# Kernel tuning notes

Measured on AMD Instinct MI355X. Metric: run time of the kernel, lower is better.

## Reference

```python
import jax, jax.numpy as jnp
import numpy as np

NUM_HEADS = 12

def setup_inputs() -> dict:
    key = jax.random.key(0)
    k1, k2, k3 = jax.random.split(key, 3)
    B, N, C = 8, 1024, 768
    x = jax.random.normal(k1, (B, N, C), dtype=jnp.float32)
    Wqkv = jax.random.normal(k2, (C, 3 * C), dtype=jnp.float32) * (C ** -0.5)
    bqkv = jnp.zeros((3 * C,), dtype=jnp.float32)
    Wproj = jax.random.normal(k3, (C, C), dtype=jnp.float32) * (C ** -0.5)
    bproj = jnp.zeros((C,), dtype=jnp.float32)
    return {"x": x, "Wqkv": Wqkv, "bqkv": bqkv, "Wproj": Wproj, "bproj": bproj}

def reference(x, Wqkv, bqkv, Wproj, bproj):
    B, N, C = x.shape
    H = NUM_HEADS
    D = C // H
    scale = D ** -0.5
    qkv = x @ Wqkv + bqkv                       # [B,N,3C]
    qkv = qkv.reshape(B, N, 3, H, D)
    q, k, v = qkv[:, :, 0], qkv[:, :, 1], qkv[:, :, 2]  # [B,N,H,D]
    attn = jnp.einsum('bnhd,bmhd->bhnm', q, k) * scale  # [B,H,N,N]
    attn = jax.nn.softmax(attn, axis=-1)
    # dropout is identity in eval mode
    out = jnp.einsum('bhnm,bmhd->bnhd', attn, v).reshape(B, N, C)
    out = out @ Wproj + bproj
    return out
```

## Files before the change

kernel.cpp:

```cpp
#include <hip/hip_runtime.h>
#include <hip/hip_bf16.h>
#include <cstdint>
#include <cstddef>

typedef __bf16 bf16;
typedef __bf16 bf16x8 __attribute__((ext_vector_type(8)));
typedef __bf16 bf16x4 __attribute__((ext_vector_type(4)));
typedef __bf16 bf16x2 __attribute__((ext_vector_type(2)));
typedef float f32x4 __attribute__((ext_vector_type(4)));
typedef float f32x16 __attribute__((ext_vector_type(16)));
typedef unsigned int u32;
typedef u32 u32x4 __attribute__((ext_vector_type(4)));

#define LDS_CAST(p) (__attribute__((address_space(3))) void*)(p)
#define GLB_CAST(p) (const __attribute__((address_space(1))) void*)(p)
#define MFMA16(a, b, c) __builtin_amdgcn_mfma_f32_16x16x32_bf16(a, b, c, 0, 0, 0)
#define MFMA32(a, b, c) __builtin_amdgcn_mfma_f32_32x32x16_bf16(a, b, c, 0, 0, 0)

#if __has_builtin(__builtin_amdgcn_exp2f)
#define EXPF(x) __builtin_amdgcn_exp2f(x)
#define QK_SCALE 0.18033688011112042f
#else
#define EXPF(x) __expf(x)
#define QK_SCALE 0.125f
#endif

static constexpr int BATCH = 8;
static constexpr int NSEQ  = 1024;
static constexpr int CDIM  = 768;
static constexpr int NH    = 12;
static constexpr int HD    = 64;
static constexpr int MTOT  = BATCH * NSEQ;
static constexpr int NC3   = 3 * CDIM;

__device__ inline u32 pkbf(float a, float b) {
    bf16x2 t = { (bf16)a, (bf16)b };
    return __builtin_bit_cast(u32, t);
}

__global__ void cast_kernel(const float* __restrict__ src, bf16* __restrict__ dst, int n4) {
    int i = blockIdx.x * blockDim.x + threadIdx.x;
    if (i < n4) {
        float4 v = ((const float4*)src)[i];
        bf16x4 o = { (bf16)v.x, (bf16)v.y, (bf16)v.z, (bf16)v.w };
        ((bf16x4*)dst)[i] = o;
    }
}

__global__ void tcast_kernel(const float* __restrict__ src, bf16* __restrict__ dst,
                             int K, int N) {
    __shared__ float tile[32][33];
    const int n0 = blockIdx.x * 32, k0 = blockIdx.y * 32;
    const int tx = threadIdx.x & 31, ty = threadIdx.x >> 5;
#pragma unroll
    for (int p = 0; p < 4; p++)
        tile[ty + p * 8][tx] = src[(size_t)(k0 + ty + p * 8) * N + n0 + tx];
    __syncthreads();
#pragma unroll
    for (int p = 0; p < 4; p++)
        dst[(size_t)(n0 + ty + p * 8) * K + k0 + tx] = (bf16)tile[tx][ty + p * 8];
}

template <int MODE>
__global__ __launch_bounds__(512, 4) void gemm_kernel(
    const bf16* __restrict__ A, const bf16* __restrict__ Bt,
    const float* __restrict__ bias, float* __restrict__ outf,
    bf16* __restrict__ q, bf16* __restrict__ kk, bf16* __restrict__ v,
    int Ndim, int K)
{
    __shared__ alignas(16) bf16 sAB[3][12288];
    const int tid  = threadIdx.x;
    const int lane = tid & 63;
    const int quad = lane >> 4;
    const int l16  = lane & 15;
    const int wid  = tid >> 6;
    const int wmI  = wid >> 1;
    const int wnI  = wid & 1;

    const int wg = blockIdx.x;
    const int x  = (wg & 7) * (gridDim.x >> 3) + (wg >> 3);
    const int nTn = Ndim >> 7;
    const int tn = x % nTn, tm = x / nTn;
    const int tmB = tm << 8, tnB = tn << 7;

    int aoff[4], boff[4];
    {
        const int xr = ((quad ^ (l16 & 3)) << 3);
#pragma unroll
        for (int i = 0; i < 4; i++) aoff[i] = (wmI * 64 + i * 16 + l16) * 32 + xr;
#pragma unroll
        for (int j = 0; j < 4; j++) boff[j] = 8192 + (wnI * 64 + j * 16 + l16) * 32 + xr;
    }

    const int r0 = tid >> 2;
    const int c0 = (tid & 3) ^ (r0 & 3);
    const bf16* gA0 = A  + (size_t)(tmB + r0) * K + c0 * 8;
    const bf16* gA1 = gA0 + (size_t)128 * K;
    const bf16* gB0 = Bt + (size_t)(tnB + r0) * K + c0 * 8;
    const int ldsb = (tid & 448) * 8;

    auto STAGE = [&](int t, int bsel) {
        const int k0 = t << 5;
        bf16* d = &sAB[bsel][0];
        __builtin_amdgcn_global_load_lds(GLB_CAST(gA0 + k0), LDS_CAST(d + ldsb),        16, 0, 0);
        __builtin_amdgcn_global_load_lds(GLB_CAST(gA1 + k0), LDS_CAST(d + 4096 + ldsb), 16, 0, 0);
        __builtin_amdgcn_global_load_lds(GLB_CAST(gB0 + k0), LDS_CAST(d + 8192 + ldsb), 16, 0, 0);
    };

    const f32x4 fzero = {0.f, 0.f, 0.f, 0.f};
    f32x4 acc[4][4];
#pragma unroll
    for (int i = 0; i < 4; i++)
#pragma unroll
        for (int j = 0; j < 4; j++) acc[i][j] = fzero;

    const int NT = K >> 5;
    STAGE(0, 0);
    STAGE(1, 1);
    asm volatile("s_waitcnt vmcnt(3)" ::: "memory");
    __builtin_amdgcn_sched_barrier(0);
    __builtin_amdgcn_s_barrier();

    int bsel = 0;
    for (int t = 0; t < NT; ++t) {
        int b2 = bsel + 2; if (b2 >= 3) b2 -= 3;
        if (t + 2 < NT) STAGE(t + 2, b2);

        const bf16* buf = &sAB[bsel][0];
        bf16x8 af[4], bfr[4];
#pragma unroll
        for (int i = 0; i < 4; i++) af[i]  = *(const bf16x8*)(buf + aoff[i]);
#pragma unroll
        for (int j = 0; j < 4; j++) bfr[j] = *(const bf16x8*)(buf + boff[j]);

        __builtin_amdgcn_s_setprio(1);
#pragma unroll
        for (int i = 0; i < 4; i++)
#pragma unroll
            for (int j = 0; j < 4; j++) acc[i][j] = MFMA16(af[i], bfr[j], acc[i][j]);
        __builtin_amdgcn_s_setprio(0);

        if (t < NT - 1) {
            if (t + 2 < NT) asm volatile("s_waitcnt vmcnt(3)" ::: "memory");
            else            asm volatile("s_waitcnt vmcnt(0)" ::: "memory");
            __builtin_amdgcn_sched_barrier(0);
            __builtin_amdgcn_s_barrier();
            __builtin_amdgcn_sched_barrier(0);
        }
        bsel += 1; if (bsel >= 3) bsel -= 3;
    }

    if (MODE == 0) {
#pragma unroll
        for (int i = 0; i < 4; i++) {
            int row = tmB + wmI * 64 + i * 16 + quad * 4;
#pragma unroll
            for (int j = 0; j < 4; j++) {
                int col = tnB + wnI * 64 + j * 16 + l16;
                float bv = bias[col];
                float* op = outf + (size_t)row * Ndim + col;
#pragma unroll
                for (int r = 0; r < 4; r++) op[(size_t)r * Ndim] = acc[i][j][r] + bv;
            }
        }
    } else {
#pragma unroll
        for (int i = 0; i < 4; i++) {
            int row = tmB + wmI * 64 + i * 16 + quad * 4;
            int b  = row >> 10;
            int ns = row & 1023;
#pragma unroll
            for (int j = 0; j < 4; j++) {
                int col = tnB + wnI * 64 + j * 16 + l16;
                int t3  = col / 768;
                int rem = col - t3 * 768;
                int h = rem >> 6;
                int d = rem & 63;
                float bv = bias[col];
                if (t3 == 0) {
                    bf16* qp = q + ((size_t)(b * NH + h) * NSEQ + ns) * HD + d;
#pragma unroll
                    for (int r = 0; r < 4; r++)
                        qp[(size_t)r * HD] = (bf16)((acc[i][j][r] + bv) * (float)QK_SCALE);
                } else if (t3 == 1) {
                    bf16* kp = kk + ((size_t)(b * NH + h) * NSEQ + ns) * HD + d;
#pragma unroll
                    for (int r = 0; r < 4; r++) kp[(size_t)r * HD] = (bf16)(acc[i][j][r] + bv);
                } else {
                    bf16x4 pv = { (bf16)(acc[i][j][0] + bv), (bf16)(acc[i][j][1] + bv),
                                  (bf16)(acc[i][j][2] + bv), (bf16)(acc[i][j][3] + bv) };
                    *(bf16x4*)(v + ((size_t)(b * NH + h) * HD + d) * NSEQ + ns) = pv;
                }
            }
        }
    }
}

__global__ __launch_bounds__(256) void attn_kernel(
    const bf16* __restrict__ q, const bf16* __restrict__ k,
    const bf16* __restrict__ v, bf16* __restrict__ o)
{
    __shared__ alignas(16) bf16 sQ[128 * 64];
    __shared__ alignas(16) bf16 sK[2][64 * 64];
    __shared__ alignas(16) bf16 sV[2][64 * 64];
    const int tid  = threadIdx.x;
    const int lane = tid & 63;
    const int w    = tid >> 6;
    const int h    = lane >> 5;
    const int l32  = lane & 31;
    const int qt = blockIdx.x;
    const int bh = blockIdx.y;
    const int b = bh / NH, hh = bh - b * NH;

    const bf16* qb = q + ((size_t)bh * NSEQ + qt * 128) * HD;
    const bf16* kb = k + (size_t)bh * NSEQ * HD;
    const bf16* vb = v + (size_t)bh * HD * NSEQ;

#pragma unroll
    for (int i = 0; i < 4; i++) {
        int slot = w * 256 + i * 64 + lane;
        int r = slot >> 3, cs = slot & 7;
        __builtin_amdgcn_global_load_lds(GLB_CAST(qb + r * HD + ((cs ^ (r & 7)) * 8)),
                                         LDS_CAST(sQ + (w * 256 + i * 64) * 8), 16, 0, 0);
    }
    auto stageKV = [&](int kt, int buf) {
#pragma unroll
        for (int i = 0; i < 2; i++) {
            int slot = w * 128 + i * 64 + lane;
            int r = slot >> 3, cs = slot & 7;
            int cc = (cs ^ (r & 7)) * 8;
            __builtin_amdgcn_global_load_lds(GLB_CAST(kb + (size_t)(kt * 64 + r) * HD + cc),
                                             LDS_CAST(&sK[buf][(w * 128 + i * 64) * 8]), 16, 0, 0);
            __builtin_amdgcn_global_load_lds(GLB_CAST(vb + (size_t)r * NSEQ + kt * 64 + cc),
                                             LDS_CAST(&sV[buf][(w * 128 + i * 64) * 8]), 16, 0, 0);
        }
    };
    stageKV(0, 0);
    __syncthreads();

    bf16x8 qf[4];
    {
        int row = w * 32 + l32, rx = row & 7;
#pragma unroll
        for (int cd = 0; cd < 4; cd++)
            qf[cd] = *(const bf16x8*)(sQ + (row * 8 + ((2 * cd + h) ^ rx)) * 8);
    }

    f32x16 accO[2];
#pragma unroll
    for (int dt = 0; dt < 2; dt++)
#pragma unroll
        for (int i = 0; i < 16; i++) accO[dt][i] = 0.f;
    float m_run = -3e38f, l_run = 0.f;

    for (int kt = 0; kt < 16; kt++) {
        const int cur = kt & 1;
        __syncthreads();
        if (kt < 15) stageKV(kt + 1, 1 - cur);
        const bf16* sKc = sK[cur];
        const bf16* sVc = sV[cur];

        f32x16 accS[2];
#pragma unroll
        for (int kvt = 0; kvt < 2; kvt++)
#pragma unroll
            for (int i = 0; i < 16; i++) accS[kvt][i] = 0.f;
#pragma unroll
        for (int kvt = 0; kvt < 2; kvt++) {
            int row = kvt * 32 + l32, rx = row & 7;
#pragma unroll
            for (int cd = 0; cd < 4; cd++) {
                bf16x8 kf = *(const bf16x8*)(sKc + (row * 8 + ((2 * cd + h) ^ rx)) * 8);
                accS[kvt] = MFMA32(kf, qf[cd], accS[kvt]);
            }
        }

        float tmv[16];
#pragma unroll
        for (int i = 0; i < 16; i++) tmv[i] = fmaxf(accS[0][i], accS[1][i]);
#pragma unroll
        for (int s = 8; s >= 1; s >>= 1)
#pragma unroll
            for (int i = 0; i < s; i++) tmv[i] = fmaxf(tmv[i], tmv[i + s]);
        float tmax = fmaxf(tmv[0], __shfl_xor(tmv[0], 32));
        float mnew = fmaxf(m_run, tmax);
        float alpha = EXPF(m_run - mnew);
        m_run = mnew;

        float tsv[16];
#pragma unroll
        for (int kvt = 0; kvt < 2; kvt++)
#pragma unroll
            for (int i = 0; i < 16; i++) {
                float p = EXPF(accS[kvt][i] - mnew);
                accS[kvt][i] = p;
            }
#pragma unroll
        for (int i = 0; i < 16; i++) tsv[i] = accS[0][i] + accS[1][i];
#pragma unroll
        for (int s = 8; s >= 1; s >>= 1)
#pragma unroll
            for (int i = 0; i < s; i++) tsv[i] += tsv[i + s];
        float rs = tsv[0] + __shfl_xor(tsv[0], 32);
        l_run = l_run * alpha + rs;
#pragma unroll
        for (int dt = 0; dt < 2; dt++)
#pragma unroll
            for (int i = 0; i < 16; i++) accO[dt][i] *= alpha;

        u32 pr[2][4][2];
#pragma unroll
        for (int kvt = 0; kvt < 2; kvt++)
#pragma unroll
            for (int g = 0; g < 4; g++) {
                pr[kvt][g][0] = pkbf(accS[kvt][4 * g + 0], accS[kvt][4 * g + 1]);
                pr[kvt][g][1] = pkbf(accS[kvt][4 * g + 2], accS[kvt][4 * g + 3]);
            }
        bf16x8 pf[4];
#pragma unroll
        for (int c = 0; c < 4; c++) {
            int kvt = c >> 1, c1 = c & 1;
            u32 u00 = pr[kvt][2 * c1][0],     u01 = pr[kvt][2 * c1][1];
            u32 u10 = pr[kvt][2 * c1 + 1][0], u11 = pr[kvt][2 * c1 + 1][1];
            u32 y0 = h ? u10 : u00, y1 = h ? u11 : u01;
            u32 z0 = h ? u00 : u10, z1 = h ? u01 : u11;
            u32 w0 = (u32)__shfl_xor((int)z0, 32);
            u32 w1 = (u32)__shfl_xor((int)z1, 32);
            u32x4 fv = { h ? w0 : y0, h ? w1 : y1, h ? y0 : w0, h ? y1 : w1 };
            pf[c] = __builtin_bit_cast(bf16x8, fv);
        }

#pragma unroll
        for (int dt = 0; dt < 2; dt++) {
            int row = dt * 32 + l32, rx = row & 7;
#pragma unroll
            for (int c = 0; c < 4; c++) {
                bf16x8 vf = *(const bf16x8*)(sVc + (row * 8 + ((2 * c + h) ^ rx)) * 8);
                accO[dt] = MFMA32(vf, pf[c], accO[dt]);
            }
        }
    }

    float inv = 1.f / l_run;
    bf16* ob = o + ((size_t)b * NSEQ + qt * 128 + w * 32 + l32) * CDIM + hh * HD;
#pragma unroll
    for (int dt = 0; dt < 2; dt++)
#pragma unroll
        for (int g = 0; g < 4; g++) {
            bf16x4 t = { (bf16)(accO[dt][4 * g + 0] * inv), (bf16)(accO[dt][4 * g + 1] * inv),
                         (bf16)(accO[dt][4 * g + 2] * inv), (bf16)(accO[dt][4 * g + 3] * inv) };
            *(bf16x4*)(ob + dt * 32 + 8 * g + 4 * h) = t;
        }
}

extern "C" void kernel_launch(void* const* d_in, const int* in_sizes, int n_in,
                              void* d_out, int out_size, void* d_ws, size_t ws_size,
                              hipStream_t stream)
{
    const float* x     = (const float*)d_in[0];
    const float* Wqkv  = (const float*)d_in[1];
    const float* bqkv  = (const float*)d_in[2];
    const float* Wproj = (const float*)d_in[3];
    const float* bproj = (const float*)d_in[4];
    float* out = (float*)d_out;

    char* ws = (char*)d_ws;
    const size_t MC2 = (size_t)MTOT * CDIM * 2;
    bf16* xb     = (bf16*)ws; ws += MC2;
    bf16* wqkvt  = (bf16*)ws; ws += (size_t)NC3 * CDIM * 2;
    bf16* wprojt = (bf16*)ws; ws += (size_t)CDIM * CDIM * 2;
    bf16* qw     = (bf16*)ws; ws += MC2;
    bf16* kw     = (bf16*)ws; ws += MC2;
    bf16* vw     = (bf16*)ws; ws += MC2;
    bf16* ow     = (bf16*)ws; ws += MC2;

    int n4 = MTOT * CDIM / 4;
    cast_kernel<<<dim3((n4 + 255) / 256), dim3(256), 0, stream>>>(x, xb, n4);
    tcast_kernel<<<dim3(NC3 / 32, CDIM / 32), dim3(256), 0, stream>>>(Wqkv,  wqkvt,  CDIM, NC3);
    tcast_kernel<<<dim3(CDIM / 32, CDIM / 32), dim3(256), 0, stream>>>(Wproj, wprojt, CDIM, CDIM);

    gemm_kernel<1><<<dim3((NC3 / 128) * (MTOT / 256)), dim3(512), 0, stream>>>(
        xb, wqkvt, bqkv, nullptr, qw, kw, vw, NC3, CDIM);

    attn_kernel<<<dim3(NSEQ / 128, BATCH * NH), dim3(256), 0, stream>>>(qw, kw, vw, ow);

    gemm_kernel<0><<<dim3((CDIM / 128) * (MTOT / 256)), dim3(512), 0, stream>>>(
        ow, wprojt, bproj, out, nullptr, nullptr, nullptr, CDIM, CDIM);
}
```

Baseline: 203.0 us.

## Shrink attention LDS, remap blocks per XCD, add lazy softmax rescale and MFMA priority

The Q tile now shares the second K/V buffer slot, cutting LDS from 48KB to 32KB so more workgroups can reside per CU. The grid is flattened and remapped so each XCD handles a contiguous set of batch-heads, which is meant to improve L2 reuse of K/V. Online softmax skips the accumulator rescale unless the wave's running max grows by more than 8 (in exp2 units). s_setprio is raised around the MFMA blocks. The lazy rescale lets unnormalised values grow to about 2^8, which is bounded but adds some risk to bf16 precision. Q reuse of buffer 1 depends on the Q fragments being read into registers before stageKV overwrites that slot.

```diff
diff --git a/kernel.cpp b/kernel.cpp
--- a/kernel.cpp
+++ b/kernel.cpp
@@ -200,16 +200,18 @@
     const bf16* __restrict__ q, const bf16* __restrict__ k,
     const bf16* __restrict__ v, bf16* __restrict__ o)
 {
-    __shared__ alignas(16) bf16 sQ[128 * 64];
-    __shared__ alignas(16) bf16 sK[2][64 * 64];
-    __shared__ alignas(16) bf16 sV[2][64 * 64];
+    __shared__ alignas(16) bf16 sKV[2][8192];
     const int tid  = threadIdx.x;
     const int lane = tid & 63;
     const int w    = tid >> 6;
     const int h    = lane >> 5;
     const int l32  = lane & 31;
-    const int qt = blockIdx.x;
-    const int bh = blockIdx.y;
+
+    const int wg  = blockIdx.x;
+    const int xcd = wg & 7;
+    const int idx = wg >> 3;
+    const int bh  = xcd * 12 + (idx % 12);
+    const int qt  = idx / 12;
     const int b = bh / NH, hh = bh - b * NH;
 
     const bf16* qb = q + ((size_t)bh * NSEQ + qt * 128) * HD;
@@ -221,7 +223,7 @@
         int slot = w * 256 + i * 64 + lane;
         int r = slot >> 3, cs = slot & 7;
         __builtin_amdgcn_global_load_lds(GLB_CAST(qb + r * HD + ((cs ^ (r & 7)) * 8)),
-                                         LDS_CAST(sQ + (w * 256 + i * 64) * 8), 16, 0, 0);
+                                         LDS_CAST(&sKV[1][(w * 256 + i * 64) * 8]), 16, 0, 0);
     }
     auto stageKV = [&](int kt, int buf) {
 #pragma unroll
@@ -230,9 +232,9 @@
             int r = slot >> 3, cs = slot & 7;
             int cc = (cs ^ (r & 7)) * 8;
             __builtin_amdgcn_global_load_lds(GLB_CAST(kb + (size_t)(kt * 64 + r) * HD + cc),
-                                             LDS_CAST(&sK[buf][(w * 128 + i * 64) * 8]), 16, 0, 0);
+                                             LDS_CAST(&sKV[buf][(w * 128 + i * 64) * 8]), 16, 0, 0);
             __builtin_amdgcn_global_load_lds(GLB_CAST(vb + (size_t)r * NSEQ + kt * 64 + cc),
-                                             LDS_CAST(&sV[buf][(w * 128 + i * 64) * 8]), 16, 0, 0);
+                                             LDS_CAST(&sKV[buf][4096 + (w * 128 + i * 64) * 8]), 16, 0, 0);
         }
     };
     stageKV(0, 0);
@@ -243,7 +245,7 @@
         int row = w * 32 + l32, rx = row & 7;
 #pragma unroll
         for (int cd = 0; cd < 4; cd++)
-            qf[cd] = *(const bf16x8*)(sQ + (row * 8 + ((2 * cd + h) ^ rx)) * 8);
+            qf[cd] = *(const bf16x8*)(&sKV[1][(row * 8 + ((2 * cd + h) ^ rx)) * 8]);
     }
 
     f32x16 accO[2];
@@ -257,14 +259,15 @@
         const int cur = kt & 1;
         __syncthreads();
         if (kt < 15) stageKV(kt + 1, 1 - cur);
-        const bf16* sKc = sK[cur];
-        const bf16* sVc = sV[cur];
+        const bf16* sKc = &sKV[cur][0];
+        const bf16* sVc = &sKV[cur][4096];
 
         f32x16 accS[2];
 #pragma unroll
         for (int kvt = 0; kvt < 2; kvt++)
 #pragma unroll
             for (int i = 0; i < 16; i++) accS[kvt][i] = 0.f;
+        __builtin_amdgcn_s_setprio(1);
 #pragma unroll
         for (int kvt = 0; kvt < 2; kvt++) {
             int row = kvt * 32 + l32, rx = row & 7;
@@ -274,6 +277,7 @@
                 accS[kvt] = MFMA32(kf, qf[cd], accS[kvt]);
             }
         }
+        __builtin_amdgcn_s_setprio(0);
 
         float tmv[16];
 #pragma unroll
@@ -283,16 +287,24 @@
 #pragma unroll
             for (int i = 0; i < s; i++) tmv[i] = fmaxf(tmv[i], tmv[i + s]);
         float tmax = fmaxf(tmv[0], __shfl_xor(tmv[0], 32));
-        float mnew = fmaxf(m_run, tmax);
-        float alpha = EXPF(m_run - mnew);
-        m_run = mnew;
+
+        if (!__all(tmax <= m_run + 8.f)) {
+            float mnew = fmaxf(m_run, tmax);
+            float alpha = EXPF(m_run - mnew);
+            m_run = mnew;
+            l_run *= alpha;
+#pragma unroll
+            for (int dt = 0; dt < 2; dt++)
+#pragma unroll
+                for (int i = 0; i < 16; i++) accO[dt][i] *= alpha;
+        }
 
         float tsv[16];
 #pragma unroll
         for (int kvt = 0; kvt < 2; kvt++)
 #pragma unroll
             for (int i = 0; i < 16; i++) {
-                float p = EXPF(accS[kvt][i] - mnew);
+                float p = EXPF(accS[kvt][i] - m_run);
                 accS[kvt][i] = p;
             }
 #pragma unroll
@@ -302,11 +314,7 @@
 #pragma unroll
             for (int i = 0; i < s; i++) tsv[i] += tsv[i + s];
         float rs = tsv[0] + __shfl_xor(tsv[0], 32);
-        l_run = l_run * alpha + rs;
-#pragma unroll
-        for (int dt = 0; dt < 2; dt++)
-#pragma unroll
-            for (int i = 0; i < 16; i++) accO[dt][i] *= alpha;
+        l_run += rs;
 
         u32 pr[2][4][2];
 #pragma unroll
@@ -330,6 +338,7 @@
             pf[c] = __builtin_bit_cast(bf16x8, fv);
         }
 
+        __builtin_amdgcn_s_setprio(1);
 #pragma unroll
         for (int dt = 0; dt < 2; dt++) {
             int row = dt * 32 + l32, rx = row & 7;
@@ -339,6 +348,7 @@
                 accO[dt] = MFMA32(vf, pf[c], accO[dt]);
             }
         }
+        __builtin_amdgcn_s_setprio(0);
     }
 
     float inv = 1.f / l_run;
@@ -382,7 +392,7 @@
     gemm_kernel<1><<<dim3((NC3 / 128) * (MTOT / 256)), dim3(512), 0, stream>>>(
         xb, wqkvt, bqkv, nullptr, qw, kw, vw, NC3, CDIM);
 
-    attn_kernel<<<dim3(NSEQ / 128, BATCH * NH), dim3(256), 0, stream>>>(qw, kw, vw, ow);
+    attn_kernel<<<dim3(768), dim3(256), 0, stream>>>(qw, kw, vw, ow);
 
     gemm_kernel<0><<<dim3((CDIM / 128) * (MTOT / 256)), dim3(512), 0, stream>>>(
         ow, wprojt, bproj, out, nullptr, nullptr, nullptr, CDIM, CDIM);
```

Measured after the change: 204.5 us. Within noise of the previous version (+0.7%).
